# Kernel tuning notes

Hardware: AMD Instinct MI355X
Metric: run time of the kernel (lower is better)

Reference implementation:

```python
import jax, jax.numpy as jnp
import numpy as np

B, SQ, SKV = 4, 2048, 2048
INPUT_DIM, EMBED_DIM, NUM_HEADS = 1024, 1024, 16
HEAD_DIM = EMBED_DIM // NUM_HEADS


def setup_inputs() -> dict:
    key = jax.random.key(0)
    kq, kc, kwkv, kwo = jax.random.split(key, 4)
    # xavier-uniform style scale for weights
    def xavier(k, shape):
        fan_in, fan_out = shape
        lim = jnp.sqrt(6.0 / (fan_in + fan_out))
        return jax.random.uniform(k, shape, jnp.float32, -lim, lim)
    return {
        "q": jax.random.normal(kq, (B, SQ, EMBED_DIM), jnp.float32),
        "c": jax.random.normal(kc, (B, SKV, INPUT_DIM), jnp.float32),
        "W_kv": xavier(kwkv, (INPUT_DIM, 2 * EMBED_DIM)),
        "b_kv": jnp.zeros((2 * EMBED_DIM,), jnp.float32),
        "W_o": xavier(kwo, (EMBED_DIM, EMBED_DIM)),
        "b_o": jnp.zeros((EMBED_DIM,), jnp.float32),
    }


def reference(q, c, W_kv, b_kv, W_o, b_o):
    Bc, Skv, _ = c.shape
    Bq, Sq, embed_dim = q.shape
    # KV projection from context: [B, Skv, 2*embed_dim]
    kv = c @ W_kv + b_kv
    kv = kv.reshape(Bc, Skv, NUM_HEADS, 2 * HEAD_DIM).transpose(0, 2, 1, 3)  # [B,H,Skv,2*hd]
    k, v = jnp.split(kv, 2, axis=-1)  # each [B,H,Skv,hd]
    # q is pre-projected; just split into heads
    qh = q.reshape(Bq, Sq, NUM_HEADS, HEAD_DIM).transpose(0, 2, 1, 3)  # [B,H,Sq,hd]
    scale = 1.0 / jnp.sqrt(jnp.asarray(HEAD_DIM, q.dtype))
    logits = jnp.einsum("bhqd,bhkd->bhqk", qh, k) * scale  # [B,H,Sq,Skv]
    attn = jax.nn.softmax(logits, axis=-1)
    values = jnp.einsum("bhqk,bhkd->bhqd", attn, v)  # [B,H,Sq,hd]
    values = values.transpose(0, 2, 1, 3).reshape(Bc, Sq, embed_dim)
    out = values @ W_o + b_o
    return out
```

## Files before the change

### kernel.cpp

```cpp
#include <hip/hip_runtime.h>

typedef __bf16 bf16x8 __attribute__((ext_vector_type(8)));
typedef float f32x4 __attribute__((ext_vector_type(4)));
typedef unsigned short u16;
typedef unsigned short u16x4 __attribute__((ext_vector_type(4)));
typedef unsigned short u16x8 __attribute__((ext_vector_type(8)));
typedef unsigned int u32x2 __attribute__((ext_vector_type(2)));

#define DEVFN __device__ __forceinline__

DEVFN u16 f32_to_bf16(float f) {
  unsigned int u = __float_as_uint(f);
  u += 0x7FFFu + ((u >> 16) & 1u);
  return (u16)(u >> 16);
}

DEVFN unsigned int cvt_pk_bf16(float a, float b) {
  unsigned int r;
  asm("v_cvt_pk_bf16_f32 %0, %1, %2" : "=v"(r) : "v"(a), "v"(b));
  return r;
}

DEVFN void load_lds16(const void* g, void* l) {
  __builtin_amdgcn_global_load_lds(
      (__attribute__((address_space(1))) void*)g,
      (__attribute__((address_space(3))) void*)l,
      16, 0, 0);
}

__global__ void cvt_cq_kernel(const float* __restrict__ c, const float* __restrict__ q,
                              u16* __restrict__ c_bf, u16* __restrict__ qh) {
  const int bid = blockIdx.x;
  if (bid < 4096) {
    int i = bid * 256 + threadIdx.x;
    const float4* p = (const float4*)c + (size_t)i * 2;
    float4 a = p[0], b = p[1];
    u16x8 o;
    o[0] = f32_to_bf16(a.x); o[1] = f32_to_bf16(a.y);
    o[2] = f32_to_bf16(a.z); o[3] = f32_to_bf16(a.w);
    o[4] = f32_to_bf16(b.x); o[5] = f32_to_bf16(b.y);
    o[6] = f32_to_bf16(b.z); o[7] = f32_to_bf16(b.w);
    *(u16x8*)(c_bf + (size_t)i * 8) = o;
  } else {
    const float SC = 0.125f * 1.44269504088896f;
    int i = (bid - 4096) * 256 + threadIdx.x;
    int dc = i & 7, sx = (i >> 3) & 2047, h = (i >> 14) & 15, b = i >> 18;
    const float4* p = (const float4*)(q + ((size_t)(b * 2048 + sx)) * 1024 + h * 64 + dc * 8);
    float4 a = p[0], bb = p[1];
    u16x8 o;
    o[0] = f32_to_bf16(a.x * SC);  o[1] = f32_to_bf16(a.y * SC);
    o[2] = f32_to_bf16(a.z * SC);  o[3] = f32_to_bf16(a.w * SC);
    o[4] = f32_to_bf16(bb.x * SC); o[5] = f32_to_bf16(bb.y * SC);
    o[6] = f32_to_bf16(bb.z * SC); o[7] = f32_to_bf16(bb.w * SC);
    *(u16x8*)(qh + (size_t)i * 8) = o;
  }
}

__global__ void transpose_w_kernel(const float* __restrict__ in, u16* __restrict__ out, int N) {
  __shared__ __align__(16) u16 T[64 * 72];
  const int tid = threadIdx.x;
  const int n0 = blockIdx.x * 64, k0 = blockIdx.y * 64;
#pragma unroll
  for (int p = 0; p < 4; ++p) {
    int l = p * 256 + tid;
    int k = l >> 4, nc = l & 15;
    const float4 v = *(const float4*)(in + (size_t)(k0 + k) * N + n0 + nc * 4);
    T[(nc * 4 + 0) * 72 + k] = f32_to_bf16(v.x);
    T[(nc * 4 + 1) * 72 + k] = f32_to_bf16(v.y);
    T[(nc * 4 + 2) * 72 + k] = f32_to_bf16(v.z);
    T[(nc * 4 + 3) * 72 + k] = f32_to_bf16(v.w);
  }
  __syncthreads();
#pragma unroll
  for (int p = 0; p < 2; ++p) {
    int u = p * 256 + tid;
    int n = u >> 3, kc = u & 7;
    u16x8 o = *(const u16x8*)(T + n * 72 + kc * 8);
    *(u16x8*)(out + (size_t)(n0 + n) * 1024 + k0 + kc * 8) = o;
  }
}

template <int MODE>
__global__ __launch_bounds__(256, 2) void gemm128(
    const u16* __restrict__ A, const u16* __restrict__ Bt,
    const float* __restrict__ bias,
    u16* __restrict__ outK, u16* __restrict__ outV,
    float* __restrict__ outF, int K) {
  __shared__ __align__(16) u16 SMEM[2 * 128 * 64];
  u16* As = SMEM;
  u16* Bs = SMEM + 128 * 64;
  const int tid = threadIdx.x;
  const int lane = tid & 63, w = tid >> 6, quad = lane >> 4, l15 = lane & 15;
  const int wm = w & 1, wn = w >> 1;
  const int tn = blockIdx.x, tm = blockIdx.y;
  const u16* Ab = A + (size_t)tm * 128 * K;
  const u16* Bb = Bt + (size_t)tn * 128 * K;

  const f32x4 zero4 = {0.f, 0.f, 0.f, 0.f};
  f32x4 acc[4][4];
#pragma unroll
  for (int mi = 0; mi < 4; ++mi)
#pragma unroll
    for (int ni = 0; ni < 4; ++ni) acc[mi][ni] = zero4;

  for (int k0 = 0; k0 < K; k0 += 64) {
#pragma unroll
    for (int p = 0; p < 4; ++p) {
      int l = p * 256 + tid;
      int r = l >> 3, dc = l & 7;
      int go = r * K + k0 + ((dc ^ (r & 7)) * 8);
      int lb = (p * 256 + (tid & 192)) * 8;
      load_lds16(Ab + go, As + lb);
      load_lds16(Bb + go, Bs + lb);
    }
    __syncthreads();
#pragma unroll
    for (int kk = 0; kk < 2; ++kk) {
      bf16x8 av[4], bv[4];
#pragma unroll
      for (int i = 0; i < 4; ++i) {
        int sw = ((kk * 4 + quad) ^ (l15 & 7)) * 8;
        av[i] = *(const bf16x8*)(As + (wm * 64 + i * 16 + l15) * 64 + sw);
        bv[i] = *(const bf16x8*)(Bs + (wn * 64 + i * 16 + l15) * 64 + sw);
      }
#pragma unroll
      for (int mi = 0; mi < 4; ++mi)
#pragma unroll
        for (int ni = 0; ni < 4; ++ni)
          acc[mi][ni] = __builtin_amdgcn_mfma_f32_16x16x32_bf16(av[mi], bv[ni], acc[mi][ni], 0, 0, 0);
    }
    __syncthreads();
  }

  if (MODE == 0) {
    const int h = tn;
    const int b = tm >> 4;
    const int sx0 = (tm & 15) * 128;
    u16* VT = SMEM;
    if (wn == 0) {
#pragma unroll
      for (int ni = 0; ni < 4; ++ni) {
        const int d = ni * 16 + l15;
        const float bb = bias[tn * 128 + d];
#pragma unroll
        for (int mi = 0; mi < 4; ++mi) {
#pragma unroll
          for (int r = 0; r < 4; ++r) {
            const int sx = sx0 + wm * 64 + mi * 16 + quad * 4 + r;
            outK[((size_t)(b * 16 + h) * 2048 + sx) * 64 + d] = f32_to_bf16(acc[mi][ni][r] + bb);
          }
        }
      }
    } else {
#pragma unroll
      for (int ni = 0; ni < 4; ++ni) {
        const int d = ni * 16 + l15;
        const float bb = bias[tn * 128 + 64 + d];
#pragma unroll
        for (int mi = 0; mi < 4; ++mi) {
          u16x4 pk;
#pragma unroll
          for (int r = 0; r < 4; ++r) pk[r] = f32_to_bf16(acc[mi][ni][r] + bb);
          *(u16x4*)(VT + d * 136 + wm * 64 + mi * 16 + quad * 4) = pk;
        }
      }
    }
    __syncthreads();
    {
      const int d = tid >> 2, ch = tid & 3;
      u16* dst = outV + (((size_t)(b * 16 + h) * 64 + d) * 2048 + sx0 + ch * 32);
      const u16* src = VT + d * 136 + ch * 32;
#pragma unroll
      for (int i = 0; i < 4; ++i)
        *(u16x8*)(dst + i * 8) = *(const u16x8*)(src + i * 8);
    }
  } else {
#pragma unroll
    for (int ni = 0; ni < 4; ++ni) {
      const int n = tn * 128 + wn * 64 + ni * 16 + l15;
      const float bb = bias[n];
#pragma unroll
      for (int mi = 0; mi < 4; ++mi) {
#pragma unroll
        for (int r = 0; r < 4; ++r) {
          const int m = tm * 128 + wm * 64 + mi * 16 + quad * 4 + r;
          outF[(size_t)m * 1024 + n] = acc[mi][ni][r] + bb;
        }
      }
    }
  }
}

__global__ __launch_bounds__(256, 5) void flash_kernel(
    const u16* __restrict__ Qh,
    const u16* __restrict__ Kp,
    const u16* __restrict__ Vt,
    u16* __restrict__ Opk) {
  __shared__ __align__(16) u16 Ks[128 * 64];
  __shared__ __align__(16) u16 Vts[64 * 128];

  const int tid = threadIdx.x;
  const int lane = tid & 63, w = tid >> 6, quad = lane >> 4, l15 = lane & 15;
  const int id = blockIdx.x;
  const int bh = (id & 7) + 8 * (id >> 8);
  const int qt = (id >> 3) & 31;
  const int q0 = qt * 64;

  const u16* kbase = Kp + (size_t)bh * 2048 * 64;
  const u16* vbase = Vt + (size_t)bh * 64 * 2048;

  const u16* qrow = Qh + ((size_t)bh * 2048 + q0 + w * 16 + l15) * 64;
  bf16x8 bq0 = *(const bf16x8*)(qrow + quad * 8);
  bf16x8 bq1 = *(const bf16x8*)(qrow + 32 + quad * 8);

  bf16x8 ones;
#pragma unroll
  for (int i = 0; i < 8; ++i) ones[i] = (__bf16)1.0f;

  const f32x4 zero4 = {0.f, 0.f, 0.f, 0.f};
  f32x4 oacc[4];
  f32x4 lacc = zero4;
#pragma unroll
  for (int di = 0; di < 4; ++di) oacc[di] = zero4;

  for (int t = 0; t < 16; ++t) {
    const int kv0 = t * 128;
#pragma unroll
    for (int p = 0; p < 4; ++p) {
      int l = p * 256 + tid;
      int kv = l >> 3, dc = l & 7;
      load_lds16(kbase + (kv0 + kv) * 64 + ((dc ^ (kv & 7)) * 8), Ks + (p * 256 + (tid & 192)) * 8);
    }
#pragma unroll
    for (int p = 0; p < 4; ++p) {
      int l = p * 256 + tid;
      int d = l >> 4, dc = l & 15;
      load_lds16(vbase + (size_t)d * 2048 + kv0 + ((dc ^ (d & 15)) * 8),
                 Vts + (p * 256 + (tid & 192)) * 8);
    }
    __syncthreads();

#pragma unroll
    for (int c = 0; c < 4; ++c) {
      f32x4 s0 = zero4, s1 = zero4;
      {
        const int sw0 = (quad ^ (l15 & 7)) * 8;
        bf16x8 ak0 = *(const bf16x8*)(Ks + ((c * 2 + 0) * 16 + l15) * 64 + sw0);
        bf16x8 ak1 = *(const bf16x8*)(Ks + ((c * 2 + 1) * 16 + l15) * 64 + sw0);
        const int sw1 = ((4 + quad) ^ (l15 & 7)) * 8;
        bf16x8 ak2 = *(const bf16x8*)(Ks + ((c * 2 + 0) * 16 + l15) * 64 + sw1);
        bf16x8 ak3 = *(const bf16x8*)(Ks + ((c * 2 + 1) * 16 + l15) * 64 + sw1);
        __builtin_amdgcn_s_setprio(1);
        s0 = __builtin_amdgcn_mfma_f32_16x16x32_bf16(ak0, bq0, s0, 0, 0, 0);
        s1 = __builtin_amdgcn_mfma_f32_16x16x32_bf16(ak1, bq0, s1, 0, 0, 0);
        s0 = __builtin_amdgcn_mfma_f32_16x16x32_bf16(ak2, bq1, s0, 0, 0, 0);
        s1 = __builtin_amdgcn_mfma_f32_16x16x32_bf16(ak3, bq1, s1, 0, 0, 0);
        __builtin_amdgcn_s_setprio(0);
      }

      f32x4 pv0, pv1;
#pragma unroll
      for (int r = 0; r < 4; ++r) {
        pv0[r] = __builtin_amdgcn_exp2f(s0[r]);
        pv1[r] = __builtin_amdgcn_exp2f(s1[r]);
      }
      unsigned int a0 = cvt_pk_bf16(pv0[0], pv0[1]);
      unsigned int a1 = cvt_pk_bf16(pv0[2], pv0[3]);
      unsigned int b0 = cvt_pk_bf16(pv1[0], pv1[1]);
      unsigned int b1 = cvt_pk_bf16(pv1[2], pv1[3]);

      u32x2 t0 = __builtin_amdgcn_permlane32_swap(a0, b0, false, false);
      u32x2 t1 = __builtin_amdgcn_permlane32_swap(a1, b1, false, false);
      u32x2 u0 = __builtin_amdgcn_permlane16_swap(t0.x, t0.y, false, false);
      u32x2 u1 = __builtin_amdgcn_permlane16_swap(t1.x, t1.y, false, false);

      union { unsigned int u[4]; bf16x8 v; } P;
      P.u[0] = u0.x;
      P.u[1] = u1.x;
      P.u[2] = u0.y;
      P.u[3] = u1.y;
      bf16x8 ap = P.v;

      bf16x8 bv0 = *(const bf16x8*)(Vts + (0 * 16 + l15) * 128 + (((c * 4 + quad) ^ l15) * 8));
      bf16x8 bv1 = *(const bf16x8*)(Vts + (1 * 16 + l15) * 128 + (((c * 4 + quad) ^ l15) * 8));
      bf16x8 bv2 = *(const bf16x8*)(Vts + (2 * 16 + l15) * 128 + (((c * 4 + quad) ^ l15) * 8));
      bf16x8 bv3 = *(const bf16x8*)(Vts + (3 * 16 + l15) * 128 + (((c * 4 + quad) ^ l15) * 8));
      __builtin_amdgcn_s_setprio(1);
      oacc[0] = __builtin_amdgcn_mfma_f32_16x16x32_bf16(ap, bv0, oacc[0], 0, 0, 0);
      oacc[1] = __builtin_amdgcn_mfma_f32_16x16x32_bf16(ap, bv1, oacc[1], 0, 0, 0);
      oacc[2] = __builtin_amdgcn_mfma_f32_16x16x32_bf16(ap, bv2, oacc[2], 0, 0, 0);
      oacc[3] = __builtin_amdgcn_mfma_f32_16x16x32_bf16(ap, bv3, oacc[3], 0, 0, 0);
      lacc = __builtin_amdgcn_mfma_f32_16x16x32_bf16(ap, ones, lacc, 0, 0, 0);
      __builtin_amdgcn_s_setprio(0);
    }
    __syncthreads();
  }

  const int b = bh >> 4, h = bh & 15;
#pragma unroll
  for (int r = 0; r < 4; ++r) {
    float linv = 1.0f / lacc[r];
    int row = q0 + w * 16 + quad * 4 + r;
    u16* dst = Opk + ((size_t)(b * 2048 + row)) * 1024 + h * 64;
#pragma unroll
    for (int di = 0; di < 4; ++di)
      dst[di * 16 + l15] = f32_to_bf16(oacc[di][r] * linv);
  }
}


extern "C" void kernel_launch(void* const* d_in, const int* in_sizes, int n_in,
                              void* d_out, int out_size, void* d_ws, size_t ws_size,
                              hipStream_t stream) {
  const float* q   = (const float*)d_in[0];
  const float* c   = (const float*)d_in[1];
  const float* Wkv = (const float*)d_in[2];
  const float* bkv = (const float*)d_in[3];
  const float* Wo  = (const float*)d_in[4];
  const float* bo  = (const float*)d_in[5];
  float* out = (float*)d_out;
  char* ws = (char*)d_ws;

  u16* c_bf = (u16*)(ws + 0);
  u16* qh   = (u16*)(ws + 16777216);
  u16* Wkvt = (u16*)(ws + 33554432);
  u16* Wot  = (u16*)(ws + 37748736);
  u16* KpB  = (u16*)(ws + 39845888);
  u16* VtB  = (u16*)(ws + 56623104);
  u16* Opk  = c_bf;

  cvt_cq_kernel<<<8192, 256, 0, stream>>>(c, q, c_bf, qh);
  transpose_w_kernel<<<dim3(32, 16), 256, 0, stream>>>(Wkv, Wkvt, 2048);
  transpose_w_kernel<<<dim3(16, 16), 256, 0, stream>>>(Wo, Wot, 1024);
  gemm128<0><<<dim3(16, 64), 256, 0, stream>>>(c_bf, Wkvt, bkv, KpB, VtB, nullptr, 1024);
  flash_kernel<<<2048, 256, 0, stream>>>(qh, KpB, VtB, Opk);
  gemm128<1><<<dim3(8, 64), 256, 0, stream>>>(Opk, Wot, bo, nullptr, nullptr, out, 1024);
}
```

Baseline: 276.7 us.

## Double-buffer K/V tiles in LDS with prefetch of next 64-key tile

Splits each 128-key K/V tile into two 64-key tiles held in a two-slot LDS ring, so the global-to-LDS loads for tile t+1 are issued before computing on tile t. Waits use explicit vmcnt counts and raw s_barrier calls instead of __syncthreads. Total LDS size stays the same, so occupancy should hold. The cost is twice as many barriers per key range and smaller tiles, and the vmcnt(4) count is hand-tuned to the number of loads issued per stage.

```diff
diff --git a/kernel.cpp b/kernel.cpp
--- a/kernel.cpp
+++ b/kernel.cpp
@@ -196,8 +196,8 @@
     const u16* __restrict__ Kp,
     const u16* __restrict__ Vt,
     u16* __restrict__ Opk) {
-  __shared__ __align__(16) u16 Ks[128 * 64];
-  __shared__ __align__(16) u16 Vts[64 * 128];
+  __shared__ __align__(16) u16 Ks[2][64 * 64];
+  __shared__ __align__(16) u16 Vts[2][64 * 64];
 
   const int tid = threadIdx.x;
   const int lane = tid & 63, w = tid >> 6, quad = lane >> 4, l15 = lane & 15;
@@ -223,33 +223,45 @@
 #pragma unroll
   for (int di = 0; di < 4; ++di) oacc[di] = zero4;
 
-  for (int t = 0; t < 16; ++t) {
-    const int kv0 = t * 128;
-#pragma unroll
-    for (int p = 0; p < 4; ++p) {
-      int l = p * 256 + tid;
-      int kv = l >> 3, dc = l & 7;
-      load_lds16(kbase + (kv0 + kv) * 64 + ((dc ^ (kv & 7)) * 8), Ks + (p * 256 + (tid & 192)) * 8);
-    }
-#pragma unroll
-    for (int p = 0; p < 4; ++p) {
-      int l = p * 256 + tid;
-      int d = l >> 4, dc = l & 15;
-      load_lds16(vbase + (size_t)d * 2048 + kv0 + ((dc ^ (d & 15)) * 8),
-                 Vts + (p * 256 + (tid & 192)) * 8);
-    }
-    __syncthreads();
-
-#pragma unroll
-    for (int c = 0; c < 4; ++c) {
+  const int skv = tid >> 3, sdc = tid & 7;
+  const int ksw = (sdc ^ (skv & 7)) * 8;
+  const int ldst = ((tid & 192) * 8);
+
+#define STAGE(tt, bi)                                                              \
+  do {                                                                             \
+    const int kv0_ = (tt)*64;                                                      \
+    load_lds16(kbase + (size_t)(kv0_ + skv) * 64 + ksw, &Ks[bi][ldst]);            \
+    load_lds16(kbase + (size_t)(kv0_ + skv + 32) * 64 + ksw, &Ks[bi][2048 + ldst]); \
+    load_lds16(vbase + (size_t)skv * 2048 + kv0_ + ksw, &Vts[bi][ldst]);           \
+    load_lds16(vbase + (size_t)(skv + 32) * 2048 + kv0_ + ksw, &Vts[bi][2048 + ldst]); \
+  } while (0)
+
+  STAGE(0, 0);
+
+  const int sw0 = (quad ^ (l15 & 7)) * 8;
+  const int sw1 = ((4 + quad) ^ (l15 & 7)) * 8;
+
+  for (int t = 0; t < 32; ++t) {
+    const int cur = t & 1;
+    if (t < 31) {
+      STAGE(t + 1, cur ^ 1);
+      asm volatile("s_waitcnt vmcnt(4)" ::: "memory");
+    } else {
+      asm volatile("s_waitcnt vmcnt(0)" ::: "memory");
+    }
+    __builtin_amdgcn_s_barrier();
+    asm volatile("" ::: "memory");
+
+    const u16* Ksb = &Ks[cur][0];
+    const u16* Vtsb = &Vts[cur][0];
+#pragma unroll
+    for (int c2 = 0; c2 < 2; ++c2) {
       f32x4 s0 = zero4, s1 = zero4;
       {
-        const int sw0 = (quad ^ (l15 & 7)) * 8;
-        bf16x8 ak0 = *(const bf16x8*)(Ks + ((c * 2 + 0) * 16 + l15) * 64 + sw0);
-        bf16x8 ak1 = *(const bf16x8*)(Ks + ((c * 2 + 1) * 16 + l15) * 64 + sw0);
-        const int sw1 = ((4 + quad) ^ (l15 & 7)) * 8;
-        bf16x8 ak2 = *(const bf16x8*)(Ks + ((c * 2 + 0) * 16 + l15) * 64 + sw1);
-        bf16x8 ak3 = *(const bf16x8*)(Ks + ((c * 2 + 1) * 16 + l15) * 64 + sw1);
+        bf16x8 ak0 = *(const bf16x8*)(Ksb + ((c2 * 2 + 0) * 16 + l15) * 64 + sw0);
+        bf16x8 ak1 = *(const bf16x8*)(Ksb + ((c2 * 2 + 1) * 16 + l15) * 64 + sw0);
+        bf16x8 ak2 = *(const bf16x8*)(Ksb + ((c2 * 2 + 0) * 16 + l15) * 64 + sw1);
+        bf16x8 ak3 = *(const bf16x8*)(Ksb + ((c2 * 2 + 1) * 16 + l15) * 64 + sw1);
         __builtin_amdgcn_s_setprio(1);
         s0 = __builtin_amdgcn_mfma_f32_16x16x32_bf16(ak0, bq0, s0, 0, 0, 0);
         s1 = __builtin_amdgcn_mfma_f32_16x16x32_bf16(ak1, bq0, s1, 0, 0, 0);
@@ -281,10 +293,10 @@
       P.u[3] = u1.y;
       bf16x8 ap = P.v;
 
-      bf16x8 bv0 = *(const bf16x8*)(Vts + (0 * 16 + l15) * 128 + (((c * 4 + quad) ^ l15) * 8));
-      bf16x8 bv1 = *(const bf16x8*)(Vts + (1 * 16 + l15) * 128 + (((c * 4 + quad) ^ l15) * 8));
-      bf16x8 bv2 = *(const bf16x8*)(Vts + (2 * 16 + l15) * 128 + (((c * 4 + quad) ^ l15) * 8));
-      bf16x8 bv3 = *(const bf16x8*)(Vts + (3 * 16 + l15) * 128 + (((c * 4 + quad) ^ l15) * 8));
+      bf16x8 bv0 = *(const bf16x8*)(Vtsb + (0 * 16 + l15) * 64 + (((c2 * 4 + quad) ^ (l15 & 7)) * 8));
+      bf16x8 bv1 = *(const bf16x8*)(Vtsb + (1 * 16 + l15) * 64 + (((c2 * 4 + quad) ^ (l15 & 7)) * 8));
+      bf16x8 bv2 = *(const bf16x8*)(Vtsb + (2 * 16 + l15) * 64 + (((c2 * 4 + quad) ^ (l15 & 7)) * 8));
+      bf16x8 bv3 = *(const bf16x8*)(Vtsb + (3 * 16 + l15) * 64 + (((c2 * 4 + quad) ^ (l15 & 7)) * 8));
       __builtin_amdgcn_s_setprio(1);
       oacc[0] = __builtin_amdgcn_mfma_f32_16x16x32_bf16(ap, bv0, oacc[0], 0, 0, 0);
       oacc[1] = __builtin_amdgcn_mfma_f32_16x16x32_bf16(ap, bv1, oacc[1], 0, 0, 0);
@@ -293,8 +305,11 @@
       lacc = __builtin_amdgcn_mfma_f32_16x16x32_bf16(ap, ones, lacc, 0, 0, 0);
       __builtin_amdgcn_s_setprio(0);
     }
-    __syncthreads();
-  }
+    asm volatile("" ::: "memory");
+    __builtin_amdgcn_s_barrier();
+    asm volatile("" ::: "memory");
+  }
+#undef STAGE
 
   const int b = bh >> 4, h = bh & 15;
 #pragma unroll
```

Result: no change. 274.9 us (-0.7%).
